# Kernel optimization log

Measured on AMD Instinct MI355X. Metric: run time of the kernel, lower is better.

The kernel has to match this reference:

```python
import jax, jax.numpy as jnp
import numpy as np

GRID_SIZE = 5   # efficient-kan default
K = 3           # spline_order
BATCH = 32768
OBS_DIM = 128
ACTION_DIM = 18
# (in_features, out_features) for the 7 KANLinear layers:
# base: 128->256->256->64 ; adv head: 64->64->18 ; value head: 64->64->1
DIMS = [(OBS_DIM, 256), (256, 256), (256, 64), (64, 64), (64, ACTION_DIM), (64, 64), (64, 1)]


def make_grid(in_f):
    # uniform grid on [-1,1] extended by K knots each side: shape (in_f, GRID_SIZE+2K+1)
    h = 2.0 / GRID_SIZE
    g = jnp.arange(-K, GRID_SIZE + K + 1, dtype=jnp.float32) * h - 1.0
    return jnp.broadcast_to(g, (in_f, g.shape[0]))


def b_splines(x, grid):
    # Cox-de Boor recursion; x: (B, in) -> bases (B, in, GRID_SIZE+K)
    xe = x[:, :, None]
    b = ((xe >= grid[:, :-1]) & (xe < grid[:, 1:])).astype(x.dtype)
    for j in range(1, K + 1):
        left = (xe - grid[:, : -(j + 1)]) / (grid[:, j:-1] - grid[:, : -(j + 1)])
        right = (grid[:, j + 1:] - xe) / (grid[:, j + 1:] - grid[:, 1:-j])
        b = left * b[:, :, :-1] + right * b[:, :, 1:]
    return b


def kan_layer(x, bw, sw, sc):
    # efficient-kan KANLinear: silu base path + spline path with standalone scaler
    grid = make_grid(x.shape[1])
    base = jax.nn.silu(x) @ bw.T                              # (B, out)
    bases = b_splines(x, grid)                                # (B, in, G+K)
    spline = jnp.einsum('big,oig->bo', bases, sw * sc[:, :, None])
    return base + spline


def setup_inputs() -> dict:
    key = jax.random.key(0)
    ks = jax.random.split(key, 1 + 3 * len(DIMS))
    inp = {"x": jax.random.normal(ks[0], (BATCH, OBS_DIM), dtype=jnp.float32)}
    for i, (fin, fout) in enumerate(DIMS):
        inp[f"bw{i}"] = jax.random.normal(ks[1 + 3 * i], (fout, fin), dtype=jnp.float32) / np.sqrt(fin).astype(np.float32)
        inp[f"sw{i}"] = jax.random.normal(ks[2 + 3 * i], (fout, fin, GRID_SIZE + K), dtype=jnp.float32) * (0.1 / np.sqrt(fin).astype(np.float32))
        inp[f"sc{i}"] = 1.0 + 0.1 * jax.random.normal(ks[3 + 3 * i], (fout, fin), dtype=jnp.float32)
    return inp


def reference(x, bw0, sw0, sc0, bw1, sw1, sc1, bw2, sw2, sc2,
              bw3, sw3, sc3, bw4, sw4, sc4, bw5, sw5, sc5, bw6, sw6, sc6):
    h = x
    for bw, sw, sc in [(bw0, sw0, sc0), (bw1, sw1, sc1), (bw2, sw2, sc2)]:
        h = kan_layer(h, bw, sw, sc)
    advantage = kan_layer(kan_layer(h, bw3, sw3, sc3), bw4, sw4, sc4)
    state_value = kan_layer(kan_layer(h, bw5, sw5, sc5), bw6, sw6, sc6)
    return (advantage, state_value)
```

## Files before the change

kernel.cpp:

```cpp
#include <hip/hip_runtime.h>

typedef unsigned short u16;
typedef unsigned int   u32;
typedef unsigned long long u64;
typedef __bf16 bf16;
typedef float f32x4  __attribute__((ext_vector_type(4)));
typedef bf16  bf16x8 __attribute__((ext_vector_type(8)));

__device__ __forceinline__ float bf2f(u16 u){ return (float)__builtin_bit_cast(bf16,u); }
__device__ __forceinline__ u16   f2bf(float f){ return __builtin_bit_cast(u16,(bf16)f); }
__device__ __forceinline__ u32   pkbf(float a,float b){ return (u32)f2bf(a)|((u32)f2bf(b)<<16); }

#define NROWS 32768

__device__ __forceinline__ uint4 basis_pk(float x)
{
  float tp  = __fmaf_rn(x, 2.5f, 5.5f);
  float tpc = fminf(fmaxf(tp, -1.0f), 12.0f);
  float fi  = floorf(tpc);
  float uu  = tpc - fi;
  int   i0  = (int)fi;
  float u2 = uu*uu, u3 = u2*uu, w1 = 1.0f-uu, w2 = w1*w1, w3 = w2*w1;
  float d1 = __fmaf_rn(3.0f, u3, __fmaf_rn(-6.0f, u2, 4.0f));
  float d2 = __fmaf_rn(3.0f, w3, __fmaf_rn(-6.0f, w2, 4.0f));
  u64 dpk = (u64)pkbf(w3, d1) | ((u64)pkbf(d2, u3) << 32);
  int ss = i0*16 - 48;
  u64 A  = dpk << (ss & 63);
  u64 Bv = dpk >> ((64-ss) & 63);
  u64 Cv = dpk << ((ss-64) & 63);
  u64 Dv = dpk >> ((-ss) & 63);
  u64 lo = (ss>=0 && ss<64)   ? A  : ((ss<0 && ss>-64) ? Dv : 0ull);
  u64 hi = (ss>=64 && ss<128) ? Cv : ((ss>0 && ss<64)  ? Bv : 0ull);
  uint4 r; r.x=(u32)lo; r.y=(u32)(lo>>32); r.z=(u32)hi; r.w=(u32)(hi>>32);
  return r;
}

__device__ __forceinline__ void expand9(float x, u16& sil, uint4& bpk)
{
  float s = x * (1.0f/(1.0f+__expf(-x)));
  sil = f2bf(s);
  bpk = basis_pk(x);
}
__device__ __forceinline__ void expand10(float x, u32& spk, uint4& bpk)
{
  float s = x * (1.0f/(1.0f+__expf(-x)));
  u16 uh = f2bf(s);
  u16 ul = f2bf(s - bf2f(uh));
  spk = (u32)uh | ((u32)ul<<16);
  bpk = basis_pk(x);
}

struct PrepArgs {
  const float* bw[7]; const float* sw[7]; const float* sc[7];
  u16* w[7];
  int cin[7]; int coutr[7]; int ntsh[7]; int fmt[7];
  u32 elems[7];
};

__global__ __launch_bounds__(256) void prep_kernel(PrepArgs pa)
{
  u32 idx = blockIdx.x*256 + threadIdx.x;
  int L = 0;
  u32 off = idx;
  while (L < 6 && off >= pa.elems[L]) { off -= pa.elems[L]; ++L; }
  int j    = off & 7;
  int lane = (off>>3) & 63;
  u32 tl   = off >> 9;
  int ntsh = pa.ntsh[L];
  u32 kstep = tl >> ntsh;
  int ntile = (int)(tl & ((1u<<ntsh)-1u));
  int o    = ntile*16 + (lane&15);
  int kpos = (lane>>4)*8 + j;
  int i = 0, g = 0; bool sil;
  if (pa.fmt[L] == 0){
    u32 c = kstep/9u; int r = (int)(kstep - c*9u);
    if (r == 0){ i = (int)c*32 + kpos; sil = true; }
    else { int kl=(r-1)*32+kpos; i=(int)c*32+(kl>>3); g=kl&7; sil = false; }
  } else {
    u32 c = kstep/5u; int r = (int)(kstep - c*5u);
    if (r == 0){ i = (int)c*16 + (kpos>>1); sil = true; }
    else { int kl=(r-1)*32+kpos; i=(int)c*16+(kl>>3); g=kl&7; sil = false; }
  }
  float v = 0.f;
  if (o < pa.coutr[L]) {
    size_t e = (size_t)o*pa.cin[L] + i;
    v = sil ? pa.bw[L][e] : pa.sw[L][e*8+g]*pa.sc[L][e]*0.16666666666666666f;
  }
  pa.w[L][off] = f2bf(v);
}

template<int CIN,int COUT,int GR,int GC,int IN_MODE,int OUT_MODE>
__global__ __launch_bounds__(512,4) void kan_layer(const void* __restrict__ hin_,
    const u16* __restrict__ W, void* __restrict__ hout_)
{
  constexpr int NCH = CIN/32;
  constexpr int TOTK = NCH*9;
  constexpr int NTILES = COUT/16;
  constexpr int MT  = 4/GR;
  constexpr int NTL = NTILES/GC;
  static_assert(GR*GC == 8, "wave grid must use all 8 waves");
  static_assert(MT*GR*16 == 64, "row coverage");
  static_assert(NTL*GC == NTILES, "col coverage");
  constexpr int SROW=20, BROW=132, BOFF=64*SROW;
  constexpr int CHUNK = BOFF + 64*BROW;
  __shared__ u32 buf[2][CHUNK];

  const int b0 = blockIdx.x*64;
  const int tid = threadIdx.x;
  const int wave = tid>>6, lane = tid&63, m = lane&15, quad = lane>>4;
  const int rg = wave / GC, cg = wave % GC;
  const int rbase = rg*(MT*16);

  const u16*   __restrict__ hb = (const u16*)hin_;
  const float* __restrict__ hf = (const float*)hin_;

  f32x4 acc[MT][NTL];
#pragma unroll
  for (int a=0;a<MT;++a)
#pragma unroll
    for (int n=0;n<NTL;++n) acc[a][n]=(f32x4){0.f,0.f,0.f,0.f};

  bf16x8 bbuf[3][NTL];
  auto loadB = [&](int kstep, bf16x8* dst){
    if (kstep < TOTK){
#pragma unroll
      for (int nt=0; nt<NTL; ++nt)
        dst[nt] = *(const bf16x8*)(W + (((size_t)kstep*NTILES + (cg*NTL+nt))*64 + lane)*8);
    }
  };
  loadB(0, bbuf[0]); loadB(1, bbuf[1]);

  float xb[2][4];
  auto loadX = [&](int kc, float* dst){
#pragma unroll
    for (int t=0;t<4;++t){
      int task = t*512+tid, row = task>>5, f = task&31;
      int gi = (b0+row)*CIN + kc*32 + f;
      dst[t] = (IN_MODE==0)? hf[gi] : bf2f(hb[gi]);
    }
  };
  auto expandChunk = [&](const float* xc, u32* dstb){
#pragma unroll
    for (int t=0;t<4;++t){
      int task=t*512+tid, row=task>>5, f=task&31;
      u16 sil; uint4 bpk;
      expand9(xc[t], sil, bpk);
      ((u16*)dstb)[row*(SROW*2) + f] = sil;
      *(uint4*)&dstb[BOFF + row*BROW + f*4] = bpk;
    }
  };

  loadX(0, xb[0]);
  expandChunk(xb[0], buf[0]);
  if (NCH > 1) loadX(1, xb[1]);
  __syncthreads();

  for (int kc=0; kc<NCH; ++kc){
    u32* cur = buf[kc&1];
    u32* nxt = buf[(kc+1)&1];
    if (kc+1 < NCH) expandChunk(xb[(kc+1)&1], nxt);
    if (kc+2 < NCH) loadX(kc+2, xb[kc&1]);
#pragma unroll
    for (int ks=0; ks<9; ++ks){
      const int kstep = kc*9 + ks;
      loadB(kstep+2, bbuf[2]);
      bf16x8 af[MT];
#pragma unroll
      for (int mt=0; mt<MT; ++mt){
        int row = rbase + mt*16 + m;
        af[mt] = (ks==0)
          ? *(const bf16x8*)&cur[row*SROW + quad*4]
          : *(const bf16x8*)&cur[BOFF + row*BROW + (ks-1)*16 + quad*4];
      }
#pragma unroll
      for (int nt=0; nt<NTL; ++nt)
#pragma unroll
        for (int mt=0; mt<MT; ++mt)
          acc[mt][nt] = __builtin_amdgcn_mfma_f32_16x16x32_bf16(af[mt], bbuf[0][nt], acc[mt][nt],0,0,0);
#pragma unroll
      for (int nt=0; nt<NTL; ++nt){ bbuf[0][nt]=bbuf[1][nt]; bbuf[1][nt]=bbuf[2][nt]; }
    }
    __syncthreads();
  }

#pragma unroll
  for (int mt=0; mt<MT; ++mt)
#pragma unroll
    for (int nt=0; nt<NTL; ++nt)
#pragma unroll
      for (int r=0; r<4; ++r){
        size_t off = (size_t)(b0 + rbase + mt*16 + quad*4 + r)*COUT + (cg*NTL+nt)*16 + m;
        if constexpr (OUT_MODE==0) ((float*)hout_)[off] = acc[mt][nt][r];
        else                       ((u16*)hout_)[off]   = f2bf(acc[mt][nt][r]);
      }
}

template<int IN_MODE>
__global__ __launch_bounds__(512,4) void tail_kernel(const void* __restrict__ h2_,
  const u16* __restrict__ W3, const u16* __restrict__ W4,
  const u16* __restrict__ W5, const u16* __restrict__ W6,
  float* __restrict__ out_adv, float* __restrict__ out_val)
{
  constexpr int SROW=20, BROW=68, BOFF=64*20;
  __shared__ u32   Aexp[BOFF + 64*BROW];
  __shared__ float hA[64*65], hV[64*65];

  const int b0 = blockIdx.x*64;
  const int tid = threadIdx.x;
  const int wave = tid>>6, lane = tid&63, m = lane&15, quad = lane>>4;
  const int rg = wave>>2, cg = wave&3;

  const u16*   __restrict__ hb = (const u16*)h2_;
  const float* __restrict__ hf = (const float*)h2_;

  f32x4 a3[2], a5[2];
#pragma unroll
  for (int mt=0;mt<2;++mt){ a3[mt]=(f32x4){0,0,0,0}; a5[mt]=(f32x4){0,0,0,0}; }

  bf16x8 w3b[3], w5b[3];
  auto loadB2 = [&](int kstep, int d){
    if (kstep < 20){
      size_t bi = (((size_t)kstep*4 + cg)*64 + lane)*8;
      w3b[d] = *(const bf16x8*)(W3+bi);
      w5b[d] = *(const bf16x8*)(W5+bi);
    }
  };
  loadB2(0,0); loadB2(1,1);

  float xb[2][2];
  auto loadX = [&](int kc, float* dst){
#pragma unroll
    for (int t=0;t<2;++t){
      int task = t*512+tid, row=task>>4, f=task&15;
      int gi = (b0+row)*64 + kc*16 + f;
      dst[t] = (IN_MODE==0)? hf[gi] : bf2f(hb[gi]);
    }
  };
  loadX(0, xb[0]);

  for (int kc=0; kc<4; ++kc){
    const float* xc = xb[kc&1];
#pragma unroll
    for (int t=0;t<2;++t){
      int task=t*512+tid, row=task>>4, f=task&15;
      u32 spk; uint4 bpk;
      expand10(xc[t], spk, bpk);
      Aexp[row*SROW + f] = spk;
      *(uint4*)&Aexp[BOFF + row*BROW + f*4] = bpk;
    }
    if (kc+1 < 4) loadX(kc+1, xb[(kc+1)&1]);
    __syncthreads();
#pragma unroll
    for (int ks=0; ks<5; ++ks){
      const int kstep = kc*5 + ks;
      loadB2(kstep+2, 2);
      bf16x8 af[2];
#pragma unroll
      for (int mt=0; mt<2; ++mt){
        int row = rg*32 + mt*16 + m;
        af[mt] = (ks==0)
          ? *(const bf16x8*)&Aexp[row*SROW + quad*4]
          : *(const bf16x8*)&Aexp[BOFF + row*BROW + (ks-1)*16 + quad*4];
      }
#pragma unroll
      for (int mt=0; mt<2; ++mt){
        a3[mt] = __builtin_amdgcn_mfma_f32_16x16x32_bf16(af[mt], w3b[0], a3[mt],0,0,0);
        a5[mt] = __builtin_amdgcn_mfma_f32_16x16x32_bf16(af[mt], w5b[0], a5[mt],0,0,0);
      }
      w3b[0]=w3b[1]; w3b[1]=w3b[2]; w5b[0]=w5b[1]; w5b[1]=w5b[2];
    }
    __syncthreads();
  }
#pragma unroll
  for (int mt=0;mt<2;++mt)
#pragma unroll
    for (int r=0;r<4;++r){
      int row = rg*32 + mt*16 + quad*4 + r;
      hA[row*65 + cg*16 + m] = a3[mt][r];
      hV[row*65 + cg*16 + m] = a5[mt][r];
    }
  __syncthreads();

  f32x4 a4[2];
#pragma unroll
  for (int mt=0;mt<2;++mt) a4[mt]=(f32x4){0,0,0,0};
  bf16x8 w4b[3];
  auto loadB4 = [&](int kstep, int d){
    if (kstep < 20) w4b[d] = *(const bf16x8*)(W4 + (((size_t)kstep*4 + cg)*64 + lane)*8);
  };
  loadB4(0,0); loadB4(1,1);
  for (int kc=0; kc<4; ++kc){
#pragma unroll
    for (int t=0;t<2;++t){
      int task=t*512+tid, row=task>>4, f=task&15;
      u32 spk; uint4 bpk;
      expand10(hA[row*65 + kc*16 + f], spk, bpk);
      Aexp[row*SROW + f] = spk;
      *(uint4*)&Aexp[BOFF + row*BROW + f*4] = bpk;
    }
    __syncthreads();
#pragma unroll
    for (int ks=0; ks<5; ++ks){
      loadB4(kc*5+ks+2, 2);
      bf16x8 af[2];
#pragma unroll
      for (int mt=0; mt<2; ++mt){
        int row = rg*32 + mt*16 + m;
        af[mt] = (ks==0)
          ? *(const bf16x8*)&Aexp[row*SROW + quad*4]
          : *(const bf16x8*)&Aexp[BOFF + row*BROW + (ks-1)*16 + quad*4];
      }
#pragma unroll
      for (int mt=0; mt<2; ++mt)
        a4[mt] = __builtin_amdgcn_mfma_f32_16x16x32_bf16(af[mt], w4b[0], a4[mt],0,0,0);
      w4b[0]=w4b[1]; w4b[1]=w4b[2];
    }
    __syncthreads();
  }
  {
    int col = cg*16 + m;
    if (col < 18){
#pragma unroll
      for (int mt=0;mt<2;++mt)
#pragma unroll
        for (int r=0;r<4;++r)
          out_adv[(size_t)(b0 + rg*32 + mt*16 + quad*4 + r)*18 + col] = a4[mt][r];
    }
  }

  f32x4 a6[2];
#pragma unroll
  for (int mt=0;mt<2;++mt) a6[mt]=(f32x4){0,0,0,0};
  bf16x8 w6b[3];
  auto loadB6 = [&](int kstep, int d){
    if (kstep < 20) w6b[d] = *(const bf16x8*)(W6 + (((size_t)kstep*4 + cg)*64 + lane)*8);
  };
  loadB6(0,0); loadB6(1,1);
  for (int kc=0; kc<4; ++kc){
#pragma unroll
    for (int t=0;t<2;++t){
      int task=t*512+tid, row=task>>4, f=task&15;
      u32 spk; uint4 bpk;
      expand10(hV[row*65 + kc*16 + f], spk, bpk);
      Aexp[row*SROW + f] = spk;
      *(uint4*)&Aexp[BOFF + row*BROW + f*4] = bpk;
    }
    __syncthreads();
#pragma unroll
    for (int ks=0; ks<5; ++ks){
      loadB6(kc*5+ks+2, 2);
      bf16x8 af[2];
#pragma unroll
      for (int mt=0; mt<2; ++mt){
        int row = rg*32 + mt*16 + m;
        af[mt] = (ks==0)
          ? *(const bf16x8*)&Aexp[row*SROW + quad*4]
          : *(const bf16x8*)&Aexp[BOFF + row*BROW + (ks-1)*16 + quad*4];
      }
#pragma unroll
      for (int mt=0; mt<2; ++mt)
        a6[mt] = __builtin_amdgcn_mfma_f32_16x16x32_bf16(af[mt], w6b[0], a6[mt],0,0,0);
      w6b[0]=w6b[1]; w6b[1]=w6b[2];
    }
    __syncthreads();
  }
  if (cg==0 && m==0){
#pragma unroll
    for (int mt=0;mt<2;++mt)
#pragma unroll
      for (int r=0;r<4;++r)
        out_val[b0 + rg*32 + mt*16 + quad*4 + r] = a6[mt][r];
  }
}

extern "C" void kernel_launch(void* const* d_in, const int* in_sizes, int n_in,
                              void* d_out, int out_size, void* d_ws, size_t ws_size,
                              hipStream_t stream)
{
  (void)in_sizes; (void)n_in; (void)out_size;
  char* ws = (char*)d_ws;

  const size_t wbytes[7] = {589824u, 1179648u, 294912u, 81920u, 81920u, 81920u, 81920u};
  const bool midf32 = ws_size >= 77889536u;

  u16* W[7];
  char *h0, *h1, *h2;
  if (midf32) {
    h0 = ws;
    h1 = h0 + 33554432u;
    h2 = h1 + 33554432u;
    size_t off = 75497472u;
    for (int l=0;l<7;++l){ W[l] = (u16*)(ws+off); off += wbytes[l]; }
  } else {
    h0 = ws;
    h1 = h0 + 16777216u;
    h2 = h1 + 16777216u;
    size_t off = 37748736u;
    for (int l=0;l<7;++l){ W[l] = (u16*)(ws+off); off += wbytes[l]; }
  }

  PrepArgs pa;
  const int cins[7]   = {128,256,256,64,64,64,64};
  const int coutr[7]  = {256,256,64,64,18,64,1};
  const int ntsh[7]   = {4,4,2,2,2,2,2};
  const int fmts[7]   = {0,0,0,1,1,1,1};
  const u32 elems[7]  = {294912u,589824u,147456u,40960u,40960u,40960u,40960u};
  for (int l=0;l<7;++l){
    pa.bw[l] = (const float*)d_in[1+3*l];
    pa.sw[l] = (const float*)d_in[2+3*l];
    pa.sc[l] = (const float*)d_in[3+3*l];
    pa.w[l]  = W[l];
    pa.cin[l]=cins[l]; pa.coutr[l]=coutr[l]; pa.ntsh[l]=ntsh[l]; pa.fmt[l]=fmts[l];
    pa.elems[l]=elems[l];
  }
  prep_kernel<<<4672, 256, 0, stream>>>(pa);

  dim3 g(NROWS/64), bl(512), bt(512);
  float* out_adv = (float*)d_out;
  float* out_val = (float*)d_out + (size_t)NROWS*18;
  if (midf32) {
    kan_layer<128,256,2,4,0,0><<<g,bl,0,stream>>>(d_in[0], W[0], h0);
    kan_layer<256,256,2,4,0,0><<<g,bl,0,stream>>>(h0, W[1], h1);
    kan_layer<256, 64,2,4,0,0><<<g,bl,0,stream>>>(h1, W[2], h2);
    tail_kernel<0><<<g,bt,0,stream>>>(h2, W[3], W[4], W[5], W[6], out_adv, out_val);
  } else {
    kan_layer<128,256,2,4,0,1><<<g,bl,0,stream>>>(d_in[0], W[0], h0);
    kan_layer<256,256,2,4,1,1><<<g,bl,0,stream>>>(h0, W[1], h1);
    kan_layer<256, 64,2,4,1,1><<<g,bl,0,stream>>>(h1, W[2], h2);
    tail_kernel<1><<<g,bt,0,stream>>>(h2, W[3], W[4], W[5], W[6], out_adv, out_val);
  }
}
```

Baseline: 238.5 us.

## Run adv/value tail heads concurrently on wave halves; retune wave grid

```diff
diff --git a/kernel.cpp b/kernel.cpp
--- a/kernel.cpp
+++ b/kernel.cpp
@@ -93,19 +93,20 @@
 __global__ __launch_bounds__(512,4) void kan_layer(const void* __restrict__ hin_,
     const u16* __restrict__ W, void* __restrict__ hout_)
 {
+  constexpr int ROWS = 64;
   constexpr int NCH = CIN/32;
   constexpr int TOTK = NCH*9;
   constexpr int NTILES = COUT/16;
-  constexpr int MT  = 4/GR;
+  constexpr int MT  = ROWS/(GR*16);
   constexpr int NTL = NTILES/GC;
   static_assert(GR*GC == 8, "wave grid must use all 8 waves");
-  static_assert(MT*GR*16 == 64, "row coverage");
+  static_assert(MT*GR*16 == ROWS, "row coverage");
   static_assert(NTL*GC == NTILES, "col coverage");
-  constexpr int SROW=20, BROW=132, BOFF=64*SROW;
-  constexpr int CHUNK = BOFF + 64*BROW;
+  constexpr int SROW=20, BROW=132, BOFF=ROWS*SROW;
+  constexpr int CHUNK = BOFF + ROWS*BROW;
   __shared__ u32 buf[2][CHUNK];
 
-  const int b0 = blockIdx.x*64;
+  const int b0 = blockIdx.x*ROWS;
   const int tid = threadIdx.x;
   const int wave = tid>>6, lane = tid&63, m = lane&15, quad = lane>>4;
   const int rg = wave / GC, cg = wave % GC;
@@ -163,7 +164,7 @@
 #pragma unroll
     for (int ks=0; ks<9; ++ks){
       const int kstep = kc*9 + ks;
-      loadB(kstep+2, bbuf[2]);
+      loadB(kstep+2, bbuf[(ks+2)%3]);
       bf16x8 af[MT];
 #pragma unroll
       for (int mt=0; mt<MT; ++mt){
@@ -176,9 +177,7 @@
       for (int nt=0; nt<NTL; ++nt)
 #pragma unroll
         for (int mt=0; mt<MT; ++mt)
-          acc[mt][nt] = __builtin_amdgcn_mfma_f32_16x16x32_bf16(af[mt], bbuf[0][nt], acc[mt][nt],0,0,0);
-#pragma unroll
-      for (int nt=0; nt<NTL; ++nt){ bbuf[0][nt]=bbuf[1][nt]; bbuf[1][nt]=bbuf[2][nt]; }
+          acc[mt][nt] = __builtin_amdgcn_mfma_f32_16x16x32_bf16(af[mt], bbuf[ks%3][nt], acc[mt][nt],0,0,0);
     }
     __syncthreads();
   }
@@ -202,7 +201,8 @@
   float* __restrict__ out_adv, float* __restrict__ out_val)
 {
   constexpr int SROW=20, BROW=68, BOFF=64*20;
-  __shared__ u32   Aexp[BOFF + 64*BROW];
+  __shared__ u32   AexpA[BOFF + 64*BROW];
+  __shared__ u32   AexpV[BOFF + 64*BROW];
   __shared__ float hA[64*65], hV[64*65];
 
   const int b0 = blockIdx.x*64;
@@ -245,8 +245,8 @@
       int task=t*512+tid, row=task>>4, f=task&15;
       u32 spk; uint4 bpk;
       expand10(xc[t], spk, bpk);
-      Aexp[row*SROW + f] = spk;
-      *(uint4*)&Aexp[BOFF + row*BROW + f*4] = bpk;
+      AexpA[row*SROW + f] = spk;
+      *(uint4*)&AexpA[BOFF + row*BROW + f*4] = bpk;
     }
     if (kc+1 < 4) loadX(kc+1, xb[(kc+1)&1]);
     __syncthreads();
@@ -259,8 +259,8 @@
       for (int mt=0; mt<2; ++mt){
         int row = rg*32 + mt*16 + m;
         af[mt] = (ks==0)
-          ? *(const bf16x8*)&Aexp[row*SROW + quad*4]
-          : *(const bf16x8*)&Aexp[BOFF + row*BROW + (ks-1)*16 + quad*4];
+          ? *(const bf16x8*)&AexpA[row*SROW + quad*4]
+          : *(const bf16x8*)&AexpA[BOFF + row*BROW + (ks-1)*16 + quad*4];
       }
 #pragma unroll
       for (int mt=0; mt<2; ++mt){
@@ -281,95 +281,65 @@
     }
   __syncthreads();
 
-  f32x4 a4[2];
-#pragma unroll
-  for (int mt=0;mt<2;++mt) a4[mt]=(f32x4){0,0,0,0};
-  bf16x8 w4b[3];
-  auto loadB4 = [&](int kstep, int d){
-    if (kstep < 20) w4b[d] = *(const bf16x8*)(W4 + (((size_t)kstep*4 + cg)*64 + lane)*8);
-  };
-  loadB4(0,0); loadB4(1,1);
+  const int half = wave>>2;
+  const float* __restrict__ hsrc = half ? hV : hA;
+  u32* __restrict__ Aex = half ? AexpV : AexpA;
+  const u16* __restrict__ Wx = half ? W6 : W4;
+
+  f32x4 ax[4];
+#pragma unroll
+  for (int mt=0;mt<4;++mt) ax[mt]=(f32x4){0,0,0,0};
+  bf16x8 wb[3];
+  auto loadBx = [&](int kstep, int d){
+    if (kstep < 20) wb[d] = *(const bf16x8*)(Wx + (((size_t)kstep*4 + cg)*64 + lane)*8);
+  };
+  loadBx(0,0); loadBx(1,1);
+
+  const int ht = tid & 255;
   for (int kc=0; kc<4; ++kc){
 #pragma unroll
-    for (int t=0;t<2;++t){
-      int task=t*512+tid, row=task>>4, f=task&15;
+    for (int t=0;t<4;++t){
+      int task = t*256 + ht, row = task>>4, f = task&15;
       u32 spk; uint4 bpk;
-      expand10(hA[row*65 + kc*16 + f], spk, bpk);
-      Aexp[row*SROW + f] = spk;
-      *(uint4*)&Aexp[BOFF + row*BROW + f*4] = bpk;
+      expand10(hsrc[row*65 + kc*16 + f], spk, bpk);
+      Aex[row*SROW + f] = spk;
+      *(uint4*)&Aex[BOFF + row*BROW + f*4] = bpk;
     }
     __syncthreads();
 #pragma unroll
     for (int ks=0; ks<5; ++ks){
-      loadB4(kc*5+ks+2, 2);
-      bf16x8 af[2];
-#pragma unroll
-      for (int mt=0; mt<2; ++mt){
-        int row = rg*32 + mt*16 + m;
+      loadBx(kc*5+ks+2, 2);
+      bf16x8 af[4];
+#pragma unroll
+      for (int mt=0; mt<4; ++mt){
+        int row = mt*16 + m;
         af[mt] = (ks==0)
-          ? *(const bf16x8*)&Aexp[row*SROW + quad*4]
-          : *(const bf16x8*)&Aexp[BOFF + row*BROW + (ks-1)*16 + quad*4];
+          ? *(const bf16x8*)&Aex[row*SROW + quad*4]
+          : *(const bf16x8*)&Aex[BOFF + row*BROW + (ks-1)*16 + quad*4];
       }
 #pragma unroll
-      for (int mt=0; mt<2; ++mt)
-        a4[mt] = __builtin_amdgcn_mfma_f32_16x16x32_bf16(af[mt], w4b[0], a4[mt],0,0,0);
-      w4b[0]=w4b[1]; w4b[1]=w4b[2];
+      for (int mt=0; mt<4; ++mt)
+        ax[mt] = __builtin_amdgcn_mfma_f32_16x16x32_bf16(af[mt], wb[0], ax[mt],0,0,0);
+      wb[0]=wb[1]; wb[1]=wb[2];
     }
     __syncthreads();
   }
-  {
+
+  if (half==0){
     int col = cg*16 + m;
     if (col < 18){
 #pragma unroll
-      for (int mt=0;mt<2;++mt)
+      for (int mt=0;mt<4;++mt)
 #pragma unroll
         for (int r=0;r<4;++r)
-          out_adv[(size_t)(b0 + rg*32 + mt*16 + quad*4 + r)*18 + col] = a4[mt][r];
-    }
-  }
-
-  f32x4 a6[2];
-#pragma unroll
-  for (int mt=0;mt<2;++mt) a6[mt]=(f32x4){0,0,0,0};
-  bf16x8 w6b[3];
-  auto loadB6 = [&](int kstep, int d){
-    if (kstep < 20) w6b[d] = *(const bf16x8*)(W6 + (((size_t)kstep*4 + cg)*64 + lane)*8);
-  };
-  loadB6(0,0); loadB6(1,1);
-  for (int kc=0; kc<4; ++kc){
-#pragma unroll
-    for (int t=0;t<2;++t){
-      int task=t*512+tid, row=task>>4, f=task&15;
-      u32 spk; uint4 bpk;
-      expand10(hV[row*65 + kc*16 + f], spk, bpk);
-      Aexp[row*SROW + f] = spk;
-      *(uint4*)&Aexp[BOFF + row*BROW + f*4] = bpk;
-    }
-    __syncthreads();
-#pragma unroll
-    for (int ks=0; ks<5; ++ks){
-      loadB6(kc*5+ks+2, 2);
-      bf16x8 af[2];
-#pragma unroll
-      for (int mt=0; mt<2; ++mt){
-        int row = rg*32 + mt*16 + m;
-        af[mt] = (ks==0)
-          ? *(const bf16x8*)&Aexp[row*SROW + quad*4]
-          : *(const bf16x8*)&Aexp[BOFF + row*BROW + (ks-1)*16 + quad*4];
-      }
-#pragma unroll
-      for (int mt=0; mt<2; ++mt)
-        a6[mt] = __builtin_amdgcn_mfma_f32_16x16x32_bf16(af[mt], w6b[0], a6[mt],0,0,0);
-      w6b[0]=w6b[1]; w6b[1]=w6b[2];
-    }
-    __syncthreads();
-  }
-  if (cg==0 && m==0){
-#pragma unroll
-    for (int mt=0;mt<2;++mt)
+          out_adv[(size_t)(b0 + mt*16 + quad*4 + r)*18 + col] = ax[mt][r];
+    }
+  } else if (cg==0 && m==0){
+#pragma unroll
+    for (int mt=0;mt<4;++mt)
 #pragma unroll
       for (int r=0;r<4;++r)
-        out_val[b0 + rg*32 + mt*16 + quad*4 + r] = a6[mt][r];
+        out_val[b0 + mt*16 + quad*4 + r] = ax[mt][r];
   }
 }
 
@@ -415,18 +385,18 @@
   }
   prep_kernel<<<4672, 256, 0, stream>>>(pa);
 
-  dim3 g(NROWS/64), bl(512), bt(512);
+  dim3 g64(NROWS/64), bl(512);
   float* out_adv = (float*)d_out;
   float* out_val = (float*)d_out + (size_t)NROWS*18;
   if (midf32) {
-    kan_layer<128,256,2,4,0,0><<<g,bl,0,stream>>>(d_in[0], W[0], h0);
-    kan_layer<256,256,2,4,0,0><<<g,bl,0,stream>>>(h0, W[1], h1);
-    kan_layer<256, 64,2,4,0,0><<<g,bl,0,stream>>>(h1, W[2], h2);
-    tail_kernel<0><<<g,bt,0,stream>>>(h2, W[3], W[4], W[5], W[6], out_adv, out_val);
+    kan_layer<128,256,1,8,0,0><<<g64,bl,0,stream>>>(d_in[0], W[0], h0);
+    kan_layer<256,256,1,8,0,0><<<g64,bl,0,stream>>>(h0, W[1], h1);
+    kan_layer<256, 64,2,4,0,0><<<g64,bl,0,stream>>>(h1, W[2], h2);
+    tail_kernel<0><<<g64,bl,0,stream>>>(h2, W[3], W[4], W[5], W[6], out_adv, out_val);
   } else {
-    kan_layer<128,256,2,4,0,1><<<g,bl,0,stream>>>(d_in[0], W[0], h0);
-    kan_layer<256,256,2,4,1,1><<<g,bl,0,stream>>>(h0, W[1], h1);
-    kan_layer<256, 64,2,4,1,1><<<g,bl,0,stream>>>(h1, W[2], h2);
-    tail_kernel<1><<<g,bt,0,stream>>>(h2, W[3], W[4], W[5], W[6], out_adv, out_val);
-  }
-}
+    kan_layer<128,256,1,8,0,1><<<g64,bl,0,stream>>>(d_in[0], W[0], h0);
+    kan_layer<256,256,1,8,1,1><<<g64,bl,0,stream>>>(h0, W[1], h1);
+    kan_layer<256, 64,2,4,1,1><<<g64,bl,0,stream>>>(h1, W[2], h2);
+    tail_kernel<1><<<g64,bl,0,stream>>>(h2, W[3], W[4], W[5], W[6], out_adv, out_val);
+  }
+}
```

Result: faster. 224.8 us (-5.7%).

## Fuse third KAN layer into tail kernel and retile wave grid

Applied to the files above, without the earlier changes.

```diff
diff --git a/kernel.cpp b/kernel.cpp
--- a/kernel.cpp
+++ b/kernel.cpp
@@ -93,19 +93,20 @@
 __global__ __launch_bounds__(512,4) void kan_layer(const void* __restrict__ hin_,
     const u16* __restrict__ W, void* __restrict__ hout_)
 {
+  constexpr int ROWS = 64;
   constexpr int NCH = CIN/32;
   constexpr int TOTK = NCH*9;
   constexpr int NTILES = COUT/16;
-  constexpr int MT  = 4/GR;
+  constexpr int MT  = ROWS/(GR*16);
   constexpr int NTL = NTILES/GC;
   static_assert(GR*GC == 8, "wave grid must use all 8 waves");
-  static_assert(MT*GR*16 == 64, "row coverage");
+  static_assert(MT*GR*16 == ROWS, "row coverage");
   static_assert(NTL*GC == NTILES, "col coverage");
-  constexpr int SROW=20, BROW=132, BOFF=64*SROW;
-  constexpr int CHUNK = BOFF + 64*BROW;
-  __shared__ u32 buf[2][CHUNK];
-
-  const int b0 = blockIdx.x*64;
+  constexpr int SROW=20, BROW=132, BOFF=ROWS*SROW;
+  constexpr int CHUNK = BOFF + ROWS*BROW;
+  __shared__ __align__(16) u32 buf[2][CHUNK];
+
+  const int b0 = blockIdx.x*ROWS;
   const int tid = threadIdx.x;
   const int wave = tid>>6, lane = tid&63, m = lane&15, quad = lane>>4;
   const int rg = wave / GC, cg = wave % GC;
@@ -163,7 +164,7 @@
 #pragma unroll
     for (int ks=0; ks<9; ++ks){
       const int kstep = kc*9 + ks;
-      loadB(kstep+2, bbuf[2]);
+      loadB(kstep+2, bbuf[(ks+2)%3]);
       bf16x8 af[MT];
 #pragma unroll
       for (int mt=0; mt<MT; ++mt){
@@ -176,9 +177,7 @@
       for (int nt=0; nt<NTL; ++nt)
 #pragma unroll
         for (int mt=0; mt<MT; ++mt)
-          acc[mt][nt] = __builtin_amdgcn_mfma_f32_16x16x32_bf16(af[mt], bbuf[0][nt], acc[mt][nt],0,0,0);
-#pragma unroll
-      for (int nt=0; nt<NTL; ++nt){ bbuf[0][nt]=bbuf[1][nt]; bbuf[1][nt]=bbuf[2][nt]; }
+          acc[mt][nt] = __builtin_amdgcn_mfma_f32_16x16x32_bf16(af[mt], bbuf[ks%3][nt], acc[mt][nt],0,0,0);
     }
     __syncthreads();
   }
@@ -196,22 +195,89 @@
 }
 
 template<int IN_MODE>
-__global__ __launch_bounds__(512,4) void tail_kernel(const void* __restrict__ h2_,
-  const u16* __restrict__ W3, const u16* __restrict__ W4,
+__global__ __launch_bounds__(512,4) void tail2_kernel(const void* __restrict__ h1_,
+  const u16* __restrict__ W2, const u16* __restrict__ W3, const u16* __restrict__ W4,
   const u16* __restrict__ W5, const u16* __restrict__ W6,
   float* __restrict__ out_adv, float* __restrict__ out_val)
 {
-  constexpr int SROW=20, BROW=68, BOFF=64*20;
-  __shared__ u32   Aexp[BOFF + 64*BROW];
-  __shared__ float hA[64*65], hV[64*65];
+  __shared__ __align__(16) u32 smem[19456];
+  float* hH = (float*)smem;
+  float* hA = (float*)(smem + 4160);
+  float* hV = (float*)(smem + 8320);
+  u32*  Aex = smem + 12480;
 
   const int b0 = blockIdx.x*64;
   const int tid = threadIdx.x;
   const int wave = tid>>6, lane = tid&63, m = lane&15, quad = lane>>4;
   const int rg = wave>>2, cg = wave&3;
 
-  const u16*   __restrict__ hb = (const u16*)h2_;
-  const float* __restrict__ hf = (const float*)h2_;
+  const u16*   __restrict__ hb = (const u16*)h1_;
+  const float* __restrict__ hf = (const float*)h1_;
+
+  {
+    constexpr int CIN=256, NCH=8, TOTK=72, NTILES=4;
+    constexpr int SROW=20, BROW=132, BOFF=64*SROW, CHUNK=BOFF+64*BROW;
+    f32x4 acc[2];
+    acc[0]=(f32x4){0,0,0,0}; acc[1]=(f32x4){0,0,0,0};
+    bf16x8 bb[3];
+    auto loadB = [&](int kstep, bf16x8* dst){
+      if (kstep < TOTK) *dst = *(const bf16x8*)(W2 + (((size_t)kstep*NTILES + cg)*64 + lane)*8);
+    };
+    loadB(0,&bb[0]); loadB(1,&bb[1]);
+    float xb[2][4];
+    auto loadX = [&](int kc, float* dst){
+#pragma unroll
+      for (int t=0;t<4;++t){
+        int task=t*512+tid, row=task>>5, f=task&31;
+        int gi=(b0+row)*CIN + kc*32 + f;
+        dst[t] = (IN_MODE==0)? hf[gi] : bf2f(hb[gi]);
+      }
+    };
+    auto expandChunk = [&](const float* xc, u32* dstb){
+#pragma unroll
+      for (int t=0;t<4;++t){
+        int task=t*512+tid, row=task>>5, f=task&31;
+        u16 sil; uint4 bpk;
+        expand9(xc[t], sil, bpk);
+        ((u16*)dstb)[row*(SROW*2)+f] = sil;
+        *(uint4*)&dstb[BOFF + row*BROW + f*4] = bpk;
+      }
+    };
+    loadX(0, xb[0]);
+    expandChunk(xb[0], smem);
+    loadX(1, xb[1]);
+    __syncthreads();
+    for (int kc=0; kc<NCH; ++kc){
+      u32* cur = smem + (kc&1)*CHUNK;
+      u32* nxt = smem + ((kc+1)&1)*CHUNK;
+      if (kc+1 < NCH) expandChunk(xb[(kc+1)&1], nxt);
+      if (kc+2 < NCH) loadX(kc+2, xb[kc&1]);
+#pragma unroll
+      for (int ks=0; ks<9; ++ks){
+        loadB(kc*9+ks+2, &bb[(ks+2)%3]);
+        bf16x8 af[2];
+#pragma unroll
+        for (int mt=0; mt<2; ++mt){
+          int row = rg*32 + mt*16 + m;
+          af[mt] = (ks==0)
+            ? *(const bf16x8*)&cur[row*SROW + quad*4]
+            : *(const bf16x8*)&cur[BOFF + row*BROW + (ks-1)*16 + quad*4];
+        }
+#pragma unroll
+        for (int mt=0; mt<2; ++mt)
+          acc[mt] = __builtin_amdgcn_mfma_f32_16x16x32_bf16(af[mt], bb[ks%3], acc[mt],0,0,0);
+      }
+      __syncthreads();
+    }
+#pragma unroll
+    for (int mt=0; mt<2; ++mt)
+#pragma unroll
+      for (int r=0;r<4;++r)
+        hH[(rg*32 + mt*16 + quad*4 + r)*65 + cg*16 + m] = acc[mt][r];
+  }
+  __syncthreads();
+
+  constexpr int SROW=20, BROW=68, BOFF=64*20;
 
   f32x4 a3[2], a5[2];
 #pragma unroll
@@ -227,28 +293,15 @@
   };
   loadB2(0,0); loadB2(1,1);
 
-  float xb[2][2];
-  auto loadX = [&](int kc, float* dst){
-#pragma unroll
-    for (int t=0;t<2;++t){
-      int task = t*512+tid, row=task>>4, f=task&15;
-      int gi = (b0+row)*64 + kc*16 + f;
-      dst[t] = (IN_MODE==0)? hf[gi] : bf2f(hb[gi]);
-    }
-  };
-  loadX(0, xb[0]);
-
   for (int kc=0; kc<4; ++kc){
-    const float* xc = xb[kc&1];
 #pragma unroll
     for (int t=0;t<2;++t){
       int task=t*512+tid, row=task>>4, f=task&15;
       u32 spk; uint4 bpk;
-      expand10(xc[t], spk, bpk);
-      Aexp[row*SROW + f] = spk;
-      *(uint4*)&Aexp[BOFF + row*BROW + f*4] = bpk;
-    }
-    if (kc+1 < 4) loadX(kc+1, xb[(kc+1)&1]);
+      expand10(hH[row*65 + kc*16 + f], spk, bpk);
+      Aex[row*SROW + f] = spk;
+      *(uint4*)&Aex[BOFF + row*BROW + f*4] = bpk;
+    }
     __syncthreads();
 #pragma unroll
     for (int ks=0; ks<5; ++ks){
@@ -259,8 +312,8 @@
       for (int mt=0; mt<2; ++mt){
         int row = rg*32 + mt*16 + m;
         af[mt] = (ks==0)
-          ? *(const bf16x8*)&Aexp[row*SROW + quad*4]
-          : *(const bf16x8*)&Aexp[BOFF + row*BROW + (ks-1)*16 + quad*4];
+          ? *(const bf16x8*)&Aex[row*SROW + quad*4]
+          : *(const bf16x8*)&Aex[BOFF + row*BROW + (ks-1)*16 + quad*4];
       }
 #pragma unroll
       for (int mt=0; mt<2; ++mt){
@@ -295,8 +348,8 @@
       int task=t*512+tid, row=task>>4, f=task&15;
       u32 spk; uint4 bpk;
       expand10(hA[row*65 + kc*16 + f], spk, bpk);
-      Aexp[row*SROW + f] = spk;
-      *(uint4*)&Aexp[BOFF + row*BROW + f*4] = bpk;
+      Aex[row*SROW + f] = spk;
+      *(uint4*)&Aex[BOFF + row*BROW + f*4] = bpk;
     }
     __syncthreads();
 #pragma unroll
@@ -307,8 +360,8 @@
       for (int mt=0; mt<2; ++mt){
         int row = rg*32 + mt*16 + m;
         af[mt] = (ks==0)
-          ? *(const bf16x8*)&Aexp[row*SROW + quad*4]
-          : *(const bf16x8*)&Aexp[BOFF + row*BROW + (ks-1)*16 + quad*4];
+          ? *(const bf16x8*)&Aex[row*SROW + quad*4]
+          : *(const bf16x8*)&Aex[BOFF + row*BROW + (ks-1)*16 + quad*4];
       }
 #pragma unroll
       for (int mt=0; mt<2; ++mt)
@@ -342,8 +395,8 @@
       int task=t*512+tid, row=task>>4, f=task&15;
       u32 spk; uint4 bpk;
       expand10(hV[row*65 + kc*16 + f], spk, bpk);
-      Aexp[row*SROW + f] = spk;
-      *(uint4*)&Aexp[BOFF + row*BROW + f*4] = bpk;
+      Aex[row*SROW + f] = spk;
+      *(uint4*)&Aex[BOFF + row*BROW + f*4] = bpk;
     }
     __syncthreads();
 #pragma unroll
@@ -354,8 +407,8 @@
       for (int mt=0; mt<2; ++mt){
         int row = rg*32 + mt*16 + m;
         af[mt] = (ks==0)
-          ? *(const bf16x8*)&Aexp[row*SROW + quad*4]
-          : *(const bf16x8*)&Aexp[BOFF + row*BROW + (ks-1)*16 + quad*4];
+          ? *(const bf16x8*)&Aex[row*SROW + quad*4]
+          : *(const bf16x8*)&Aex[BOFF + row*BROW + (ks-1)*16 + quad*4];
       }
 #pragma unroll
       for (int mt=0; mt<2; ++mt)
@@ -384,17 +437,15 @@
   const bool midf32 = ws_size >= 77889536u;
 
   u16* W[7];
-  char *h0, *h1, *h2;
+  char *h0, *h1;
   if (midf32) {
     h0 = ws;
     h1 = h0 + 33554432u;
-    h2 = h1 + 33554432u;
     size_t off = 75497472u;
     for (int l=0;l<7;++l){ W[l] = (u16*)(ws+off); off += wbytes[l]; }
   } else {
     h0 = ws;
     h1 = h0 + 16777216u;
-    h2 = h1 + 16777216u;
     size_t off = 37748736u;
     for (int l=0;l<7;++l){ W[l] = (u16*)(ws+off); off += wbytes[l]; }
   }
@@ -415,18 +466,16 @@
   }
   prep_kernel<<<4672, 256, 0, stream>>>(pa);
 
-  dim3 g(NROWS/64), bl(512), bt(512);
+  dim3 g64(NROWS/64), bl(512);
   float* out_adv = (float*)d_out;
   float* out_val = (float*)d_out + (size_t)NROWS*18;
   if (midf32) {
-    kan_layer<128,256,2,4,0,0><<<g,bl,0,stream>>>(d_in[0], W[0], h0);
-    kan_layer<256,256,2,4,0,0><<<g,bl,0,stream>>>(h0, W[1], h1);
-    kan_layer<256, 64,2,4,0,0><<<g,bl,0,stream>>>(h1, W[2], h2);
-    tail_kernel<0><<<g,bt,0,stream>>>(h2, W[3], W[4], W[5], W[6], out_adv, out_val);
+    kan_layer<128,256,1,8,0,0><<<g64,bl,0,stream>>>(d_in[0], W[0], h0);
+    kan_layer<256,256,1,8,0,0><<<g64,bl,0,stream>>>(h0, W[1], h1);
+    tail2_kernel<0><<<g64,bl,0,stream>>>(h1, W[2], W[3], W[4], W[5], W[6], out_adv, out_val);
   } else {
-    kan_layer<128,256,2,4,0,1><<<g,bl,0,stream>>>(d_in[0], W[0], h0);
-    kan_layer<256,256,2,4,1,1><<<g,bl,0,stream>>>(h0, W[1], h1);
-    kan_layer<256, 64,2,4,1,1><<<g,bl,0,stream>>>(h1, W[2], h2);
-    tail_kernel<1><<<g,bt,0,stream>>>(h2, W[3], W[4], W[5], W[6], out_adv, out_val);
-  }
-}
+    kan_layer<128,256,1,8,0,1><<<g64,bl,0,stream>>>(d_in[0], W[0], h0);
+    kan_layer<256,256,1,8,1,1><<<g64,bl,0,stream>>>(h0, W[1], h1);
+    tail2_kernel<1><<<g64,bl,0,stream>>>(h1, W[2], W[3], W[4], W[5], W[6], out_adv, out_val);
+  }
+}
```

After: 220.7 us. 1.08x faster.
